# Optimization experiments

Hardware: AMD Instinct MI355X
Metric: run time of the kernel (lower is better)

Reference implementation:

```python
import jax, jax.numpy as jnp
import numpy as np

IGNORE_INDEX = -100
LABEL_SMOOTHING = 0.0


def setup_inputs() -> dict:
    key = jax.random.key(0)
    k1, k2, k3, k4 = jax.random.split(key, 4)
    BT, H, V = 4096, 1024, 32000
    x = jax.random.normal(k1, (BT, H), dtype=jnp.float32)
    target = jax.random.randint(k2, (BT,), 0, V, dtype=jnp.int64)
    # scale weight so logits have O(1) std (realistic trained lm_head scale)
    weight = jax.random.normal(k3, (V, H), dtype=jnp.float32) * 0.02
    bias = jax.random.normal(k4, (V,), dtype=jnp.float32) * 0.02
    return {"x": x, "target": target, "weight": weight, "bias": bias}


def reference(x, target, weight, bias):
    # x: [BT, H], weight: [V, H], bias: [V], target: [BT]
    V = weight.shape[0]
    ls = LABEL_SMOOTHING
    logits = x @ weight.T + bias                     # [BT, V]
    lse = jax.nn.logsumexp(logits, axis=-1)          # [BT]
    # gather logit at the target class (clip so ignore_index rows stay in-bounds)
    safe_t = jnp.clip(target, 0, V - 1)
    x_y = jnp.take_along_axis(logits, safe_t[:, None], axis=-1)[:, 0]
    # CE with label smoothing: (1-ls)*(lse - x_y) + ls*lse - (ls/V)*sum_j x_j
    per_row = (1.0 - ls) * (lse - x_y)
    if ls > 0.0:
        per_row = per_row + ls * lse - (ls / V) * jnp.sum(logits, axis=-1)
    valid = target != IGNORE_INDEX
    per_row = jnp.where(valid, per_row, 0.0)
    n_non_ignore = jnp.sum(valid).astype(per_row.dtype)
    loss = jnp.sum(per_row) / n_non_ignore
    return loss
```

## Files before the change

kernel.cpp:

```cpp
#include <hip/hip_runtime.h>
#include <hip/hip_bf16.h>
#include <stdint.h>


typedef float f16v __attribute__((ext_vector_type(16)));
typedef int v8i __attribute__((ext_vector_type(8)));

__device__ __forceinline__ unsigned pk_fp8(float4 v) {
  int w = 0;
  w = __builtin_amdgcn_cvt_pk_fp8_f32(v.x, v.y, w, false);
  w = __builtin_amdgcn_cvt_pk_fp8_f32(v.z, v.w, w, true);
  return (unsigned)w;
}

__global__ __launch_bounds__(256) void cast_swz_k(const float* __restrict__ in,
                                                  uint4* __restrict__ out,
                                                  long n16) {
  long t = (long)blockIdx.x * blockDim.x + threadIdx.x;
  long stride = (long)gridDim.x * blockDim.x;
  for (; t < n16; t += stride) {
    long o = t * 16;
    int c = (int)(o >> 11);
    int rem = (int)(o & 2047);
    int h = rem >> 10;
    int lam = (rem >> 4) & 63;
    int row = (c >> 4) * 32 + (lam & 31);
    int k = (c & 15) * 64 + (lam >> 5) * 32 + h * 16;
    const float4* src = (const float4*)(in + (long)row * 1024 + k);
    uint4 oo;
    oo.x = pk_fp8(src[0]); oo.y = pk_fp8(src[1]);
    oo.z = pk_fp8(src[2]); oo.w = pk_fp8(src[3]);
    out[t] = oo;
  }
}

__global__ __launch_bounds__(256) void xy_k(const float* __restrict__ x,
                                            const float* __restrict__ w,
                                            const float* __restrict__ bias,
                                            const int* __restrict__ tgt,
                                            float* __restrict__ xy, int H, int V) {
  int row = blockIdx.x;
  int t = tgt[row];
  int st = min(max(t, 0), V - 1);
  const float4* xr = (const float4*)(x + (long)row * H);
  const float4* wr = (const float4*)(w + (long)st * H);
  float s = 0.f;
  int n4 = H >> 2;
  for (int i = threadIdx.x; i < n4; i += 256) {
    float4 a = xr[i], b = wr[i];
    s += a.x * b.x + a.y * b.y + a.z * b.z + a.w * b.w;
  }
  for (int off = 32; off; off >>= 1) s += __shfl_down(s, off, 64);
  __shared__ float sm[4];
  if ((threadIdx.x & 63) == 0) sm[threadIdx.x >> 6] = s;
  __syncthreads();
  if (threadIdx.x == 0) xy[row] = sm[0] + sm[1] + sm[2] + sm[3] + bias[st];
}

__global__ __launch_bounds__(256, 2)
void gemm_sumexp(const char* __restrict__ Xf, const char* __restrict__ Wf,
                 const float* __restrict__ bias, float* __restrict__ partials,
                 int H, int BT) {
  __shared__ float rowsum[2][256];

  const int tid = threadIdx.x;
  const int w = tid >> 6, lane = tid & 63;
  const int wr = w >> 1, wc = w & 1;
  const int l32 = lane & 31, kh = lane >> 5;
  const int m0 = blockIdx.x * 256, n0 = blockIdx.y * 128;

  f16v acc[4][2];
#pragma unroll
  for (int mi = 0; mi < 4; mi++)
#pragma unroll
    for (int ni = 0; ni < 2; ni++)
#pragma unroll
      for (int r = 0; r < 16; r++) acc[mi][ni][r] = 0.f;

  const int Rb = blockIdx.x * 8 + wr * 4;
  const int Nb = blockIdx.y * 4 + wc * 2;

  const char* pa[4];
  const char* pb[2];
#pragma unroll
  for (int mi = 0; mi < 4; mi++)
    pa[mi] = Xf + ((long)(Rb + mi) * 16) * 2048 + lane * 16;
#pragma unroll
  for (int ni = 0; ni < 2; ni++)
    pb[ni] = Wf + ((long)(Nb + ni) * 16) * 2048 + lane * 16;

  const int nG = H >> 6;
#pragma unroll 4
  for (int g = 0; g < nG; g++) {
    v8i a[4], b[2];
#pragma unroll
    for (int mi = 0; mi < 4; mi++) {
      int4 lo = *(const int4*)(pa[mi]);
      int4 hi = *(const int4*)(pa[mi] + 1024);
      v8i t;
      t[0] = lo.x; t[1] = lo.y; t[2] = lo.z; t[3] = lo.w;
      t[4] = hi.x; t[5] = hi.y; t[6] = hi.z; t[7] = hi.w;
      a[mi] = t;
      pa[mi] += 2048;
    }
#pragma unroll
    for (int ni = 0; ni < 2; ni++) {
      int4 lo = *(const int4*)(pb[ni]);
      int4 hi = *(const int4*)(pb[ni] + 1024);
      v8i t;
      t[0] = lo.x; t[1] = lo.y; t[2] = lo.z; t[3] = lo.w;
      t[4] = hi.x; t[5] = hi.y; t[6] = hi.z; t[7] = hi.w;
      b[ni] = t;
      pb[ni] += 2048;
    }
#pragma unroll
    for (int mi = 0; mi < 4; mi++)
#pragma unroll
      for (int ni = 0; ni < 2; ni++)
        acc[mi][ni] = __builtin_amdgcn_mfma_scale_f32_32x32x64_f8f6f4(
            a[mi], b[ni], acc[mi][ni], 0 , 0 ,
            0, 127 , 0, 127 );
  }

  float bv[2];
  bv[0] = bias[n0 + wc * 64 + l32];
  bv[1] = bias[n0 + wc * 64 + 32 + l32];

#pragma unroll
  for (int mi = 0; mi < 4; mi++) {
    float p[16];
#pragma unroll
    for (int r = 0; r < 16; r++) p[r] = 0.f;
#pragma unroll
    for (int ni = 0; ni < 2; ni++)
#pragma unroll
      for (int r = 0; r < 16; r++) p[r] += __expf(acc[mi][ni][r] + bv[ni]);
#pragma unroll
    for (int off = 1; off < 32; off <<= 1)
#pragma unroll
      for (int r = 0; r < 16; r++) p[r] += __shfl_xor(p[r], off, 32);
    if (l32 == 0) {
#pragma unroll
      for (int r = 0; r < 16; r++)
        rowsum[wc][wr * 128 + mi * 32 + (r & 3) + 8 * (r >> 2) + 4 * kh] = p[r];
    }
  }
  __syncthreads();
  partials[(long)blockIdx.y * BT + m0 + tid] = rowsum[0][tid] + rowsum[1][tid];
}

__global__ __launch_bounds__(256)
void row_reduce(const float* __restrict__ partials, const float* __restrict__ xy,
                const int* __restrict__ tgt, float* __restrict__ bsum,
                float* __restrict__ bcnt, int BT, int nCB) {
  int row = blockIdx.x * 256 + threadIdx.x;
  float S = 0.f;
  for (int b = 0; b < nCB; b++) S += partials[(long)b * BT + row];
  int t = tgt[row];
  bool valid = (t != -100);
  float pr = valid ? (logf(S) - xy[row]) : 0.f;
  float c = valid ? 1.f : 0.f;
  for (int off = 32; off; off >>= 1) {
    pr += __shfl_down(pr, off, 64);
    c += __shfl_down(c, off, 64);
  }
  __shared__ float sp[4], sc[4];
  if ((threadIdx.x & 63) == 0) {
    sp[threadIdx.x >> 6] = pr;
    sc[threadIdx.x >> 6] = c;
  }
  __syncthreads();
  if (threadIdx.x == 0) {
    bsum[blockIdx.x] = sp[0] + sp[1] + sp[2] + sp[3];
    bcnt[blockIdx.x] = sc[0] + sc[1] + sc[2] + sc[3];
  }
}

__global__ void finalize(const float* __restrict__ bsum, const float* __restrict__ bcnt,
                         float* __restrict__ out, int nb) {
  float s = 0.f, c = 0.f;
  for (int i = threadIdx.x; i < nb; i += 64) { s += bsum[i]; c += bcnt[i]; }
  for (int off = 32; off; off >>= 1) {
    s += __shfl_down(s, off, 64);
    c += __shfl_down(c, off, 64);
  }
  if (threadIdx.x == 0) out[0] = s / c;
}

extern "C" void kernel_launch(void* const* d_in, const int* in_sizes, int n_in,
                              void* d_out, int out_size, void* d_ws, size_t ws_size,
                              hipStream_t stream) {
  const float* x = (const float*)d_in[0];
  const int* tgt = (const int*)d_in[1];
  const float* w = (const float*)d_in[2];
  const float* bias = (const float*)d_in[3];
  float* out = (float*)d_out;

  const int BT = in_sizes[1];
  const int V = in_sizes[3];
  const int H = in_sizes[0] / BT;
  const int nCB = V / 128;

  char* ws = (char*)d_ws;
  const long wb_bytes = (long)V * H;
  const long xb_bytes = (long)BT * H;
  char* Wf = ws;
  char* Xf = ws + wb_bytes;
  float* partials = (float*)(ws + wb_bytes + xb_bytes);
  float* xy = partials + (long)nCB * BT;
  float* bsum = xy + BT;
  float* bcnt = bsum + (BT / 256);

  cast_swz_k<<<8192, 256, 0, stream>>>(w, (uint4*)Wf, (long)V * H / 16);
  cast_swz_k<<<1024, 256, 0, stream>>>(x, (uint4*)Xf, (long)BT * H / 16);
  xy_k<<<BT, 256, 0, stream>>>(x, w, bias, tgt, xy, H, V);
  dim3 grid(BT / 256, nCB);
  gemm_sumexp<<<grid, 256, 0, stream>>>(Xf, Wf, bias, partials, H, BT);
  row_reduce<<<BT / 256, 256, 0, stream>>>(partials, xy, tgt, bsum, bcnt, BT, nCB);
  finalize<<<1, 64, 0, stream>>>(bsum, bcnt, out, BT / 256);
}
```

Baseline: 423.8 us.

## Double-buffer GEMM operands in LDS via async global loads, swizzle blocks, parallelize row reduce

The GEMM now stages each 64-wide k-slice of the fp8 X and W tiles into a double-buffered LDS region using global_load_lds. The next slice is prefetched while MFMAs run on the current one, so the whole block shares each tile instead of every wave loading its own operands straight from global memory. Workgroup IDs are remapped in groups of eight to improve L2 locality, and MFMA issue priority is raised. The row reduction now splits each row's partial-sum loop across four threads to get more parallelism. The cost is two barriers per k-step and 48KB of LDS per block, which may limit occupancy.

```diff
diff --git a/kernel.cpp b/kernel.cpp
--- a/kernel.cpp
+++ b/kernel.cpp
@@ -57,17 +57,52 @@
   if (threadIdx.x == 0) xy[row] = sm[0] + sm[1] + sm[2] + sm[3] + bias[st];
 }
 
+#define LDS_BUF 24576
+
 __global__ __launch_bounds__(256, 2)
 void gemm_sumexp(const char* __restrict__ Xf, const char* __restrict__ Wf,
                  const float* __restrict__ bias, float* __restrict__ partials,
                  int H, int BT) {
+  __shared__ char lds[2 * LDS_BUF];
   __shared__ float rowsum[2][256];
 
   const int tid = threadIdx.x;
   const int w = tid >> 6, lane = tid & 63;
   const int wr = w >> 1, wc = w & 1;
   const int l32 = lane & 31, kh = lane >> 5;
-  const int m0 = blockIdx.x * 256, n0 = blockIdx.y * 128;
+
+  const int nbx = gridDim.x;
+  const int nwg = nbx * gridDim.y;
+  const int id = blockIdx.y * nbx + blockIdx.x;
+  const int swz = ((nwg & 7) == 0) ? ((id & 7) * (nwg >> 3) + (id >> 3)) : id;
+  const int bx = swz % nbx;
+  const int by = swz / nbx;
+  const int m0 = bx * 256, n0 = by * 128;
+
+  const char* segsrc[6];
+  int segdst[6];
+#pragma unroll
+  for (int r = 0; r < 6; ++r) {
+    const int s = w * 6 + r;
+    if (s < 16) {
+      long base = (long)(bx * 8 + (s >> 1)) * 32768 + (long)(s & 1) * 1024;
+      segsrc[r] = Xf + base + lane * 16;
+    } else {
+      long base = (long)(by * 4 + ((s - 16) >> 1)) * 32768 + (long)((s - 16) & 1) * 1024;
+      segsrc[r] = Wf + base + lane * 16;
+    }
+    segdst[r] = s * 1024;
+  }
+
+  auto STAGE = [&](int g) {
+    const int bo = (g & 1) * LDS_BUF;
+#pragma unroll
+    for (int r = 0; r < 6; ++r)
+      __builtin_amdgcn_global_load_lds(
+          (const __attribute__((address_space(1))) void*)(segsrc[r] + (long)g * 2048),
+          (__attribute__((address_space(3))) void*)(lds + bo + segdst[r]),
+          16, 0, 0);
+  };
 
   f16v acc[4][2];
 #pragma unroll
@@ -77,42 +112,38 @@
 #pragma unroll
       for (int r = 0; r < 16; r++) acc[mi][ni][r] = 0.f;
 
-  const int Rb = blockIdx.x * 8 + wr * 4;
-  const int Nb = blockIdx.y * 4 + wc * 2;
-
-  const char* pa[4];
-  const char* pb[2];
-#pragma unroll
-  for (int mi = 0; mi < 4; mi++)
-    pa[mi] = Xf + ((long)(Rb + mi) * 16) * 2048 + lane * 16;
-#pragma unroll
-  for (int ni = 0; ni < 2; ni++)
-    pb[ni] = Wf + ((long)(Nb + ni) * 16) * 2048 + lane * 16;
-
   const int nG = H >> 6;
-#pragma unroll 4
-  for (int g = 0; g < nG; g++) {
+
+  STAGE(0);
+  STAGE(1);
+  asm volatile("s_waitcnt vmcnt(6)" ::: "memory");
+  __builtin_amdgcn_s_barrier();
+
+#pragma unroll 2
+  for (int g = 0; g < nG; ++g) {
+    const int bo = (g & 1) * LDS_BUF;
     v8i a[4], b[2];
 #pragma unroll
     for (int mi = 0; mi < 4; mi++) {
-      int4 lo = *(const int4*)(pa[mi]);
-      int4 hi = *(const int4*)(pa[mi] + 1024);
+      const char* p = lds + bo + (wr * 4 + mi) * 2048 + lane * 16;
+      int4 lo = *(const int4*)(p);
+      int4 hi = *(const int4*)(p + 1024);
       v8i t;
       t[0] = lo.x; t[1] = lo.y; t[2] = lo.z; t[3] = lo.w;
       t[4] = hi.x; t[5] = hi.y; t[6] = hi.z; t[7] = hi.w;
       a[mi] = t;
-      pa[mi] += 2048;
     }
 #pragma unroll
     for (int ni = 0; ni < 2; ni++) {
-      int4 lo = *(const int4*)(pb[ni]);
-      int4 hi = *(const int4*)(pb[ni] + 1024);
+      const char* p = lds + bo + 16384 + (wc * 2 + ni) * 2048 + lane * 16;
+      int4 lo = *(const int4*)(p);
+      int4 hi = *(const int4*)(p + 1024);
       v8i t;
       t[0] = lo.x; t[1] = lo.y; t[2] = lo.z; t[3] = lo.w;
       t[4] = hi.x; t[5] = hi.y; t[6] = hi.z; t[7] = hi.w;
       b[ni] = t;
-      pb[ni] += 2048;
-    }
+    }
+    __builtin_amdgcn_s_setprio(1);
 #pragma unroll
     for (int mi = 0; mi < 4; mi++)
 #pragma unroll
@@ -120,6 +151,16 @@
         acc[mi][ni] = __builtin_amdgcn_mfma_scale_f32_32x32x64_f8f6f4(
             a[mi], b[ni], acc[mi][ni], 0 , 0 ,
             0, 127 , 0, 127 );
+    __builtin_amdgcn_s_setprio(0);
+
+    __builtin_amdgcn_s_barrier();
+    if (g + 2 < nG) {
+      STAGE(g + 2);
+      asm volatile("s_waitcnt vmcnt(6)" ::: "memory");
+    } else {
+      asm volatile("s_waitcnt vmcnt(0)" ::: "memory");
+    }
+    __builtin_amdgcn_s_barrier();
   }
 
   float bv[2];
@@ -146,20 +187,24 @@
     }
   }
   __syncthreads();
-  partials[(long)blockIdx.y * BT + m0 + tid] = rowsum[0][tid] + rowsum[1][tid];
+  partials[(long)by * BT + m0 + tid] = rowsum[0][tid] + rowsum[1][tid];
 }
 
 __global__ __launch_bounds__(256)
 void row_reduce(const float* __restrict__ partials, const float* __restrict__ xy,
                 const int* __restrict__ tgt, float* __restrict__ bsum,
                 float* __restrict__ bcnt, int BT, int nCB) {
-  int row = blockIdx.x * 256 + threadIdx.x;
+  const int row = blockIdx.x * 64 + (threadIdx.x >> 2);
+  const int q = threadIdx.x & 3;
   float S = 0.f;
-  for (int b = 0; b < nCB; b++) S += partials[(long)b * BT + row];
-  int t = tgt[row];
-  bool valid = (t != -100);
-  float pr = valid ? (logf(S) - xy[row]) : 0.f;
-  float c = valid ? 1.f : 0.f;
+  for (int b = q; b < nCB; b += 4) S += partials[(long)b * BT + row];
+  S += __shfl_xor(S, 1, 64);
+  S += __shfl_xor(S, 2, 64);
+  float pr = 0.f, c = 0.f;
+  if (q == 0) {
+    int t = tgt[row];
+    if (t != -100) { pr = logf(S) - xy[row]; c = 1.f; }
+  }
   for (int off = 32; off; off >>= 1) {
     pr += __shfl_down(pr, off, 64);
     c += __shfl_down(c, off, 64);
@@ -209,13 +254,13 @@
   float* partials = (float*)(ws + wb_bytes + xb_bytes);
   float* xy = partials + (long)nCB * BT;
   float* bsum = xy + BT;
-  float* bcnt = bsum + (BT / 256);
+  float* bcnt = bsum + (BT / 64);
 
   cast_swz_k<<<8192, 256, 0, stream>>>(w, (uint4*)Wf, (long)V * H / 16);
   cast_swz_k<<<1024, 256, 0, stream>>>(x, (uint4*)Xf, (long)BT * H / 16);
   xy_k<<<BT, 256, 0, stream>>>(x, w, bias, tgt, xy, H, V);
   dim3 grid(BT / 256, nCB);
   gemm_sumexp<<<grid, 256, 0, stream>>>(Xf, Wf, bias, partials, H, BT);
-  row_reduce<<<BT / 256, 256, 0, stream>>>(partials, xy, tgt, bsum, bcnt, BT, nCB);
-  finalize<<<1, 64, 0, stream>>>(bsum, bcnt, out, BT / 256);
-}
+  row_reduce<<<BT / 64, 256, 0, stream>>>(partials, xy, tgt, bsum, bcnt, BT, nCB);
+  finalize<<<1, 64, 0, stream>>>(bsum, bcnt, out, BT / 64);
+}
```

Result: faster. 389.9 us (-8.0%).

## Remap GEMM blocks per XCD for L2 reuse and widen row reduction

Applied to the files above, without the earlier changes.

The GEMM grid is remapped so consecutive blocks dispatched round-robin to each of the 8 XCDs share contiguous row tiles. Blocks on one XCD then reuse X tiles in that XCD's L2. Separately, row_reduce now uses 4 threads per row, each summing a strided quarter of the 250 column partials, combined with shuffles. This launches 4x more blocks to raise parallelism in the reduction. The remap relies on the assumed round-robin XCD dispatch order.

```diff
diff --git a/kernel.cpp b/kernel.cpp
--- a/kernel.cpp
+++ b/kernel.cpp
@@ -67,7 +67,21 @@
   const int w = tid >> 6, lane = tid & 63;
   const int wr = w >> 1, wc = w & 1;
   const int l32 = lane & 31, kh = lane >> 5;
-  const int m0 = blockIdx.x * 256, n0 = blockIdx.y * 128;
+
+  const int nbx = gridDim.x;
+  const int d = blockIdx.y * nbx + blockIdx.x;
+  int bx, by;
+  if ((nbx & 7) == 0) {
+    const int sl = nbx >> 3;
+    const int xcd = d & 7;
+    const int j = d >> 3;
+    bx = xcd * sl + (j % sl);
+    by = j / sl;
+  } else {
+    bx = blockIdx.x;
+    by = blockIdx.y;
+  }
+  const int m0 = bx * 256, n0 = by * 128;
 
   f16v acc[4][2];
 #pragma unroll
@@ -77,8 +91,8 @@
 #pragma unroll
       for (int r = 0; r < 16; r++) acc[mi][ni][r] = 0.f;
 
-  const int Rb = blockIdx.x * 8 + wr * 4;
-  const int Nb = blockIdx.y * 4 + wc * 2;
+  const int Rb = bx * 8 + wr * 4;
+  const int Nb = by * 4 + wc * 2;
 
   const char* pa[4];
   const char* pb[2];
@@ -146,20 +160,24 @@
     }
   }
   __syncthreads();
-  partials[(long)blockIdx.y * BT + m0 + tid] = rowsum[0][tid] + rowsum[1][tid];
+  partials[(long)by * BT + m0 + tid] = rowsum[0][tid] + rowsum[1][tid];
 }
 
 __global__ __launch_bounds__(256)
 void row_reduce(const float* __restrict__ partials, const float* __restrict__ xy,
                 const int* __restrict__ tgt, float* __restrict__ bsum,
                 float* __restrict__ bcnt, int BT, int nCB) {
-  int row = blockIdx.x * 256 + threadIdx.x;
+  const int row = blockIdx.x * 64 + (threadIdx.x >> 2);
+  const int q = threadIdx.x & 3;
   float S = 0.f;
-  for (int b = 0; b < nCB; b++) S += partials[(long)b * BT + row];
-  int t = tgt[row];
-  bool valid = (t != -100);
-  float pr = valid ? (logf(S) - xy[row]) : 0.f;
-  float c = valid ? 1.f : 0.f;
+  for (int b = q; b < nCB; b += 4) S += partials[(long)b * BT + row];
+  S += __shfl_xor(S, 1, 64);
+  S += __shfl_xor(S, 2, 64);
+  float pr = 0.f, c = 0.f;
+  if (q == 0) {
+    int t = tgt[row];
+    if (t != -100) { pr = logf(S) - xy[row]; c = 1.f; }
+  }
   for (int off = 32; off; off >>= 1) {
     pr += __shfl_down(pr, off, 64);
     c += __shfl_down(c, off, 64);
@@ -209,13 +227,13 @@
   float* partials = (float*)(ws + wb_bytes + xb_bytes);
   float* xy = partials + (long)nCB * BT;
   float* bsum = xy + BT;
-  float* bcnt = bsum + (BT / 256);
+  float* bcnt = bsum + (BT / 64);
 
   cast_swz_k<<<8192, 256, 0, stream>>>(w, (uint4*)Wf, (long)V * H / 16);
   cast_swz_k<<<1024, 256, 0, stream>>>(x, (uint4*)Xf, (long)BT * H / 16);
   xy_k<<<BT, 256, 0, stream>>>(x, w, bias, tgt, xy, H, V);
   dim3 grid(BT / 256, nCB);
   gemm_sumexp<<<grid, 256, 0, stream>>>(Xf, Wf, bias, partials, H, BT);
-  row_reduce<<<BT / 256, 256, 0, stream>>>(partials, xy, tgt, bsum, bcnt, BT, nCB);
-  finalize<<<1, 64, 0, stream>>>(bsum, bcnt, out, BT / 256);
-}
+  row_reduce<<<BT / 64, 256, 0, stream>>>(partials, xy, tgt, bsum, bcnt, BT, nCB);
+  finalize<<<1, 64, 0, stream>>>(bsum, bcnt, out, BT / 64);
+}
```

Result: faster. 380.2 us (-10.3%).
